# Performance work log

Hardware: AMD Instinct MI355X
Metric: run time of the kernel (lower is better)

Reference implementation:

```python
import jax, jax.numpy as jnp
import numpy as np

EMBED_DIM = 1024
NUM_HEADS = 16
BATCH = 4
SEQ = 4096


def setup_inputs() -> dict:
    key = jax.random.key(0)
    ks = jax.random.split(key, 5)
    scale = 0.02
    E = EMBED_DIM
    x = jax.random.normal(ks[0], (BATCH, SEQ, E), dtype=jnp.float32)
    Wq = jax.random.normal(ks[1], (E, E), dtype=jnp.float32) * scale
    Wk = jax.random.normal(ks[2], (E, E), dtype=jnp.float32) * scale
    Wv = jax.random.normal(ks[3], (E, E), dtype=jnp.float32) * scale
    Wo = jax.random.normal(ks[4], (E, E), dtype=jnp.float32) * scale
    z = jnp.zeros((E,), dtype=jnp.float32)
    return {"x": x, "Wq": Wq, "bq": z, "Wk": Wk, "bk": z, "Wv": Wv, "bv": z, "Wo": Wo, "bo": z}


def reference(x, Wq, bq, Wk, bk, Wv, bv, Wo, bo):
    B, S, E = x.shape
    H = NUM_HEADS
    D = E // H
    # torch nn.Linear: y = x @ W.T + b
    def proj(W, b):
        return (jnp.einsum('bse,fe->bsf', x, W) + b).reshape(B, S, H, D)
    q = jax.nn.elu(proj(Wq, bq)) + 1.0  # [B,S,H,D] feature map
    k = jax.nn.elu(proj(Wk, bk)) + 1.0
    v = proj(Wv, bv)
    # kv aggregation over sequence: [B,H,D,D]
    kv = jnp.einsum('bshd,bshe->bhde', k, v)
    # Q . KV: [B,S,H,D] -> merge heads -> [B,S,E]
    out = jnp.einsum('bshd,bhde->bshe', q, kv).reshape(B, S, E)
    # output projection (dropout is identity at inference)
    out = jnp.einsum('bse,fe->bsf', out, Wo) + bo
    return out
```

## Files before the change

### kernel.cpp

```cpp
#include <hip/hip_runtime.h>
#include <hip/hip_bf16.h>
#include <cstdint>
#include <cstddef>

#define BATCH 4
#define SEQ   4096
#define EMB   1024
#define M_TOT (BATCH * SEQ)
#define KV_CHUNKS 16

using bf16_t = __hip_bfloat16;
typedef __attribute__((ext_vector_type(8))) short bv8;
typedef __attribute__((ext_vector_type(4))) float f32x4;

union SV8 { bv8 v; bf16_t h[8]; };

__device__ __forceinline__ void gload_lds16(const void* g, void* l) {
  __builtin_amdgcn_global_load_lds(
      (const __attribute__((address_space(1))) unsigned int*)g,
      (__attribute__((address_space(3))) unsigned int*)l, 16, 0, 0);
}

#define BAR() asm volatile("s_barrier" ::: "memory")

__global__ __launch_bounds__(256) void cvt_kernel(const float* __restrict__ in,
                                                  bf16_t* __restrict__ out) {
  const size_t i = ((size_t)blockIdx.x * 256 + threadIdx.x) * 8;
  const f32x4 a = *(const f32x4*)(in + i);
  const f32x4 b = *(const f32x4*)(in + i + 4);
  SV8 o;
#pragma unroll
  for (int j = 0; j < 4; ++j) o.h[j] = __float2bfloat16(a[j]);
#pragma unroll
  for (int j = 0; j < 4; ++j) o.h[4 + j] = __float2bfloat16(b[j]);
  *(bv8*)(out + i) = o.v;
}

__global__ __launch_bounds__(256) void wcvt_kernel(
    const float* __restrict__ s0, const float* __restrict__ s1,
    const float* __restrict__ s2, const float* __restrict__ s3,
    bf16_t* __restrict__ d0, bf16_t* __restrict__ d1,
    bf16_t* __restrict__ d2, bf16_t* __restrict__ d3) {
  const float* in; bf16_t* out;
  switch (blockIdx.y) {
    case 0:  in = s0; out = d0; break;
    case 1:  in = s1; out = d1; break;
    case 2:  in = s2; out = d2; break;
    default: in = s3; out = d3; break;
  }
  const size_t i = ((size_t)blockIdx.x * 256 + threadIdx.x) * 8;
  const f32x4 a = *(const f32x4*)(in + i);
  const f32x4 b = *(const f32x4*)(in + i + 4);
  SV8 o;
#pragma unroll
  for (int j = 0; j < 4; ++j) o.h[j] = __float2bfloat16(a[j]);
#pragma unroll
  for (int j = 0; j < 4; ++j) o.h[4 + j] = __float2bfloat16(b[j]);
  *(bv8*)(out + i) = o.v;
}

template <int VARIANT>
__global__ __launch_bounds__(512, 2) void gemm8p(
    const bf16_t* __restrict__ A, const bf16_t* __restrict__ Wbase,
    const float* __restrict__ b0, const float* __restrict__ b1,
    const float* __restrict__ b2, void* __restrict__ o0,
    void* __restrict__ o1, void* __restrict__ o2) {
  constexpr int K = 1024;
  constexpr int NT = (VARIANT == 0) ? 12 : 4;
  constexpr int NKT = K / 64;
  __shared__ char lds[131072];

  const int nwg = NT * 64;
  const int wg = (blockIdx.x & 7) * (nwg >> 3) + (blockIdx.x >> 3);
  const int m0 = (wg / NT) * 256;
  const int n0 = (wg % NT) * 256;
  const bf16_t* W = Wbase + (VARIANT ? (size_t)(m0 >> 12) * 1048576ull : 0);
  const int t = threadIdx.x, l = t & 63, w = t >> 6;
  const int wm = w >> 2, wn = w & 3;

  const int sr = ((t >> 7) << 4) + (t & 15);
  const int sc = (((t >> 6) & 1) << 5) + (((t >> 4) & 3) << 3);
  const bf16_t* aRow = A + (size_t)(m0 + sr) * K + sc;
  const bf16_t* wRow = W + (size_t)(n0 + sr) * K + sc;
  char* dA = lds + t * 16;
  char* dB = lds + 65536 + t * 16;

  auto ST = [&](int isB, int hf, int kt) {
    char* d = (isB ? dB : dA) + (kt & 1) * 32768 + hf * 16384;
    const bf16_t* s = (isB ? wRow : aRow) + (size_t)(hf * 128) * K + kt * 64;
    gload_lds16(s, d);
    gload_lds16(s + (size_t)64 * K, d + 8192);
  };

  const char* Ab = lds + wm * 16384 + l * 16;
  const char* Bb = lds + 65536 + (wn >> 1) * 16384 + (wn & 1) * 8192 + l * 16;

  f32x4 acc[8][4] = {};
  bv8 af[4][2], bf[4][2];

  ST(1, 0, 0); ST(1, 1, 0); ST(0, 0, 0); ST(0, 1, 0);
  ST(1, 0, 1); ST(1, 1, 1); ST(0, 0, 1);
  asm volatile("s_waitcnt vmcnt(6)" ::: "memory");
  BAR();

#pragma unroll 1
  for (int j = 0; j < NKT; ++j) {
    const int db = (j & 1) * 32768;
#pragma unroll
    for (int mb = 0; mb < 4; ++mb)
#pragma unroll
      for (int ks = 0; ks < 2; ++ks)
        af[mb][ks] = *(const bv8*)(Ab + db + mb * 2048 + ks * 1024);
#pragma unroll
    for (int nb = 0; nb < 4; ++nb)
#pragma unroll
      for (int ks = 0; ks < 2; ++ks)
        bf[nb][ks] = *(const bv8*)(Bb + db + nb * 2048 + ks * 1024);
    if (j + 1 < NKT) ST(0, 1, j + 1);
    BAR();
    __builtin_amdgcn_s_setprio(1);
#pragma unroll
    for (int mb = 0; mb < 4; ++mb)
#pragma unroll
      for (int nb = 0; nb < 2; ++nb)
#pragma unroll
        for (int ks = 0; ks < 2; ++ks)
          acc[mb][nb] = __builtin_amdgcn_mfma_f32_16x16x32_bf16(
              af[mb][ks], bf[nb][ks], acc[mb][nb], 0, 0, 0);
    __builtin_amdgcn_s_setprio(0);
    BAR();
    if (j + 2 < NKT) ST(1, 0, j + 2);
    BAR();
    __builtin_amdgcn_s_setprio(1);
#pragma unroll
    for (int mb = 0; mb < 4; ++mb)
#pragma unroll
      for (int nb = 2; nb < 4; ++nb)
#pragma unroll
        for (int ks = 0; ks < 2; ++ks)
          acc[mb][nb] = __builtin_amdgcn_mfma_f32_16x16x32_bf16(
              af[mb][ks], bf[nb][ks], acc[mb][nb], 0, 0, 0);
    __builtin_amdgcn_s_setprio(0);
    BAR();
#pragma unroll
    for (int mb = 0; mb < 4; ++mb)
#pragma unroll
      for (int ks = 0; ks < 2; ++ks)
        af[mb][ks] = *(const bv8*)(Ab + db + 8192 + mb * 2048 + ks * 1024);
    if (j + 2 < NKT) ST(1, 1, j + 2);
    BAR();
    __builtin_amdgcn_s_setprio(1);
#pragma unroll
    for (int mb = 0; mb < 4; ++mb)
#pragma unroll
      for (int nb = 2; nb < 4; ++nb)
#pragma unroll
        for (int ks = 0; ks < 2; ++ks)
          acc[4 + mb][nb] = __builtin_amdgcn_mfma_f32_16x16x32_bf16(
              af[mb][ks], bf[nb][ks], acc[4 + mb][nb], 0, 0, 0);
    __builtin_amdgcn_s_setprio(0);
    BAR();
    if (j + 2 < NKT) {
      ST(0, 0, j + 2);
      asm volatile("s_waitcnt vmcnt(6)" ::: "memory");
    } else if (j == NKT - 2) {
      asm volatile("s_waitcnt vmcnt(0)" ::: "memory");
    }
    BAR();
    __builtin_amdgcn_s_setprio(1);
#pragma unroll
    for (int mb = 0; mb < 4; ++mb)
#pragma unroll
      for (int nb = 0; nb < 2; ++nb)
#pragma unroll
        for (int ks = 0; ks < 2; ++ks)
          acc[4 + mb][nb] = __builtin_amdgcn_mfma_f32_16x16x32_bf16(
              af[mb][ks], bf[nb][ks], acc[4 + mb][nb], 0, 0, 0);
    __builtin_amdgcn_s_setprio(0);
    BAR();
  }

  const int cr = (l >> 4) << 2, cc = l & 15;
  if (VARIANT == 0) {
    const int gq = n0 >> 10;
    const float* bias = gq == 0 ? b0 : (gq == 1 ? b1 : b2);
    bf16_t* ob = (bf16_t*)(gq == 0 ? o0 : (gq == 1 ? o1 : o2));
    const int cb = (n0 & 1023) + wn * 64;
#pragma unroll
    for (int nb = 0; nb < 4; ++nb) {
      const int col = cb + nb * 16 + cc;
      const float bz = bias[col];
#pragma unroll
      for (int mb = 0; mb < 8; ++mb) {
        const int row = m0 + wm * 128 + mb * 16 + cr;
#pragma unroll
        for (int r = 0; r < 4; ++r) {
          float v = acc[mb][nb][r] + bz;
          if (gq < 2) v = (v > 0.f) ? (v + 1.f) : __expf(v);
          ob[(size_t)(row + r) * 1024 + col] = __float2bfloat16(v);
        }
      }
    }
  } else {
    const int cb = n0 + wn * 64;
#pragma unroll
    for (int nb = 0; nb < 4; ++nb) {
      const int col = cb + nb * 16 + cc;
      const float bz = b0[col];
#pragma unroll
      for (int mb = 0; mb < 8; ++mb) {
        const int row = m0 + wm * 128 + mb * 16 + cr;
#pragma unroll
        for (int r = 0; r < 4; ++r)
          ((float*)o0)[(size_t)(row + r) * 1024 + col] = acc[mb][nb][r] + bz;
      }
    }
  }
}

__global__ __launch_bounds__(256) void kv_partial(const bf16_t* __restrict__ Kmat,
                                                  const bf16_t* __restrict__ Vmat,
                                                  float* __restrict__ pkv) {
  const int chunk = blockIdx.x;
  const int bh = blockIdx.y;
  const int b = bh >> 4, h = bh & 15;
  const int t = threadIdx.x;
  __shared__ bf16_t kl[8][64], vl[8][64];
  float acc[16] = {};
  const int e = t & 63, d0 = (t >> 6) * 16;
  const int sl = t >> 5, c2 = (t & 31) * 2;
  const int s0 = chunk * (SEQ / KV_CHUNKS);
  const bf16_t* kp = Kmat + ((size_t)(b * SEQ + s0 + sl)) * EMB + h * 64 + c2;
  const bf16_t* vp = Vmat + ((size_t)(b * SEQ + s0 + sl)) * EMB + h * 64 + c2;
  for (int it = 0; it < (SEQ / KV_CHUNKS) / 8; ++it) {
    const unsigned int kw = *(const unsigned int*)kp;
    const unsigned int vw = *(const unsigned int*)vp;
    __syncthreads();
    *(unsigned int*)&kl[sl][c2] = kw;
    *(unsigned int*)&vl[sl][c2] = vw;
    __syncthreads();
#pragma unroll
    for (int ss = 0; ss < 8; ++ss) {
      const float vv = __bfloat162float(vl[ss][e]);
      SV8 k0, k1;
      k0.v = *(const bv8*)&kl[ss][d0];
      k1.v = *(const bv8*)&kl[ss][d0 + 8];
#pragma unroll
      for (int dd = 0; dd < 8; ++dd) acc[dd] += __bfloat162float(k0.h[dd]) * vv;
#pragma unroll
      for (int dd = 0; dd < 8; ++dd) acc[8 + dd] += __bfloat162float(k1.h[dd]) * vv;
    }
    kp += 8 * EMB;
    vp += 8 * EMB;
  }
  float* outp = pkv + ((size_t)chunk * 64 + bh) * 4096;
#pragma unroll
  for (int dd = 0; dd < 16; ++dd) outp[(d0 + dd) * 64 + e] = acc[dd];
}

__global__ __launch_bounds__(256) void kv_reduce(const float* __restrict__ pkv,
                                                 bf16_t* __restrict__ kvf) {
  const int bh = blockIdx.x;
  const int t = threadIdx.x;
#pragma unroll
  for (int ii = 0; ii < 16; ++ii) {
    const int idx = ii * 256 + t;
    float s = 0.f;
#pragma unroll
    for (int c = 0; c < KV_CHUNKS; ++c)
      s += pkv[((size_t)c * 64 + bh) * 4096 + idx];
    kvf[(size_t)bh * 4096 + idx] = __float2bfloat16(s);
  }
}

__global__ __launch_bounds__(256) void fold_kernel(const bf16_t* __restrict__ Wo,
                                                   const bf16_t* __restrict__ kvf,
                                                   bf16_t* __restrict__ MT) {
  __shared__ char lds[24576];
  const int ft = blockIdx.x;
  const int bh = blockIdx.y;
  const int b = bh >> 4, h = bh & 15;
  const int t = threadIdx.x, l = t & 63, w = t >> 6;
#pragma unroll
  for (int q = 0; q < 4; ++q) {
    const int s = q * 256 + t;
    const int row = ((s >> 7) << 4) + (s & 15);
    const int col = (((s >> 6) & 1) << 5) + (((s >> 4) & 3) << 3);
    gload_lds16(Wo + (size_t)(ft * 128 + row) * 1024 + h * 64 + col, lds + s * 16);
  }
#pragma unroll
  for (int q = 0; q < 2; ++q) {
    const int s = q * 256 + t;
    const int row = ((s >> 7) << 4) + (s & 15);
    const int col = (((s >> 6) & 1) << 5) + (((s >> 4) & 3) << 3);
    gload_lds16(kvf + (size_t)bh * 4096 + row * 64 + col, lds + 16384 + s * 16);
  }
  asm volatile("s_waitcnt vmcnt(0)" ::: "memory");
  BAR();
  f32x4 acc[2][4] = {};
#pragma unroll
  for (int ks = 0; ks < 2; ++ks) {
    bv8 am[2], bn[4];
#pragma unroll
    for (int i = 0; i < 2; ++i)
      am[i] = *(const bv8*)(lds + (w * 2 + i) * 2048 + ks * 1024 + l * 16);
#pragma unroll
    for (int nb = 0; nb < 4; ++nb)
      bn[nb] = *(const bv8*)(lds + 16384 + nb * 2048 + ks * 1024 + l * 16);
#pragma unroll
    for (int i = 0; i < 2; ++i)
#pragma unroll
      for (int nb = 0; nb < 4; ++nb)
        acc[i][nb] = __builtin_amdgcn_mfma_f32_16x16x32_bf16(am[i], bn[nb],
                                                             acc[i][nb], 0, 0, 0);
  }
  bf16_t* out = MT + (size_t)b * 1048576ull;
  const int cr = (l >> 4) << 2, cc = l & 15;
#pragma unroll
  for (int i = 0; i < 2; ++i)
#pragma unroll
    for (int nb = 0; nb < 4; ++nb)
#pragma unroll
      for (int r = 0; r < 4; ++r)
        out[(size_t)(ft * 128 + w * 32 + i * 16 + cr + r) * 1024 + h * 64 +
            nb * 16 + cc] = __float2bfloat16(acc[i][nb][r]);
}

extern "C" void kernel_launch(void* const* d_in, const int* in_sizes, int n_in,
                              void* d_out, int out_size, void* d_ws, size_t ws_size,
                              hipStream_t stream) {
  (void)in_sizes; (void)n_in; (void)out_size;
  const float* x  = (const float*)d_in[0];
  const float* Wq = (const float*)d_in[1];
  const float* bq = (const float*)d_in[2];
  const float* Wk = (const float*)d_in[3];
  const float* bk = (const float*)d_in[4];
  const float* Wv = (const float*)d_in[5];
  const float* bv = (const float*)d_in[6];
  const float* Wo = (const float*)d_in[7];
  const float* bo = (const float*)d_in[8];

  const size_t NEED = 72ull * 1024 * 1024;
  if (ws_size < NEED) return;

  char* p = (char*)d_ws;
  bf16_t* xb   = (bf16_t*)p;
  float*  pkv  = (float*)p;
  bf16_t* kvf  = (bf16_t*)(p + 16777216ull);
  bf16_t* MT   = (bf16_t*)(p + 17825792ull);
  bf16_t* wqkv = (bf16_t*)(p + 33554432ull);
  bf16_t* wob  = (bf16_t*)(p + 39845888ull);
  bf16_t* qb   = (bf16_t*)(p + 41943040ull);

  bf16_t* kb = (bf16_t*)d_out;
  bf16_t* vb = kb + 16777216ull;

  cvt_kernel<<<8192, 256, 0, stream>>>(x, xb);
  wcvt_kernel<<<dim3(512, 4), 256, 0, stream>>>(
      Wq, Wk, Wv, Wo, wqkv, wqkv + 1048576, wqkv + 2097152, wob);

  gemm8p<0><<<768, 512, 0, stream>>>(xb, wqkv, bq, bk, bv, qb, kb, vb);

  kv_partial<<<dim3(KV_CHUNKS, 64), 256, 0, stream>>>(kb, vb, pkv);
  kv_reduce<<<64, 256, 0, stream>>>(pkv, kvf);
  fold_kernel<<<dim3(8, 64), 256, 0, stream>>>(wob, kvf, MT);

  gemm8p<1><<<256, 512, 0, stream>>>(qb, MT, bo, nullptr, nullptr,
                                     d_out, nullptr, nullptr);
}
```

Baseline: 389.7 us.

## Fuse conversion kernels, merge kv reduce into fold, vectorize GEMM epilogue stores

Merges the x and weight fp32-to-bf16 conversions into a single launch, and fuses the KV chunk reduction into the Wo fold kernel so the reduced KV matrix stays in LDS instead of going through global memory. It swaps the MFMA operand order so each lane holds four consecutive columns, which lets the GEMM epilogues use 4-wide vector stores and vector bias loads instead of scalar strided stores. The cost is that the fold now runs on only 64 blocks that loop serially over 8 output tiles, which lowers parallelism for that stage.

```diff
diff --git a/kernel.cpp b/kernel.cpp
--- a/kernel.cpp
+++ b/kernel.cpp
@@ -12,8 +12,16 @@
 using bf16_t = __hip_bfloat16;
 typedef __attribute__((ext_vector_type(8))) short bv8;
 typedef __attribute__((ext_vector_type(4))) float f32x4;
+typedef __attribute__((ext_vector_type(4))) unsigned short us4;
 
 union SV8 { bv8 v; bf16_t h[8]; };
+
+static __device__ __forceinline__ unsigned short bfbits(float v) {
+  bf16_t b = __float2bfloat16(v);
+  unsigned short u;
+  __builtin_memcpy(&u, &b, 2);
+  return u;
+}
 
 __device__ __forceinline__ void gload_lds16(const void* g, void* l) {
   __builtin_amdgcn_global_load_lds(
@@ -23,32 +31,28 @@
 
 #define BAR() asm volatile("s_barrier" ::: "memory")
 
-__global__ __launch_bounds__(256) void cvt_kernel(const float* __restrict__ in,
-                                                  bf16_t* __restrict__ out) {
-  const size_t i = ((size_t)blockIdx.x * 256 + threadIdx.x) * 8;
-  const f32x4 a = *(const f32x4*)(in + i);
-  const f32x4 b = *(const f32x4*)(in + i + 4);
-  SV8 o;
-#pragma unroll
-  for (int j = 0; j < 4; ++j) o.h[j] = __float2bfloat16(a[j]);
-#pragma unroll
-  for (int j = 0; j < 4; ++j) o.h[4 + j] = __float2bfloat16(b[j]);
-  *(bv8*)(out + i) = o.v;
-}
-
-__global__ __launch_bounds__(256) void wcvt_kernel(
-    const float* __restrict__ s0, const float* __restrict__ s1,
-    const float* __restrict__ s2, const float* __restrict__ s3,
-    bf16_t* __restrict__ d0, bf16_t* __restrict__ d1,
-    bf16_t* __restrict__ d2, bf16_t* __restrict__ d3) {
-  const float* in; bf16_t* out;
-  switch (blockIdx.y) {
-    case 0:  in = s0; out = d0; break;
-    case 1:  in = s1; out = d1; break;
-    case 2:  in = s2; out = d2; break;
-    default: in = s3; out = d3; break;
-  }
-  const size_t i = ((size_t)blockIdx.x * 256 + threadIdx.x) * 8;
+__global__ __launch_bounds__(256) void cvt_all(
+    const float* __restrict__ x, const float* __restrict__ wq,
+    const float* __restrict__ wk, const float* __restrict__ wv,
+    const float* __restrict__ wo, bf16_t* __restrict__ xb,
+    bf16_t* __restrict__ wqkv, bf16_t* __restrict__ wob) {
+  const int bid = blockIdx.x;
+  const float* in;
+  bf16_t* out;
+  size_t base;
+  if (bid < 8192) {
+    in = x; out = xb; base = (size_t)bid * 2048;
+  } else {
+    const int q = (bid - 8192) >> 9, sub = (bid - 8192) & 511;
+    base = (size_t)sub * 2048;
+    switch (q) {
+      case 0:  in = wq; out = wqkv; break;
+      case 1:  in = wk; out = wqkv + 1048576; break;
+      case 2:  in = wv; out = wqkv + 2097152; break;
+      default: in = wo; out = wob; break;
+    }
+  }
+  const size_t i = base + (size_t)threadIdx.x * 8;
   const f32x4 a = *(const f32x4*)(in + i);
   const f32x4 b = *(const f32x4*)(in + i + 4);
   SV8 o;
@@ -126,7 +130,7 @@
 #pragma unroll
         for (int ks = 0; ks < 2; ++ks)
           acc[mb][nb] = __builtin_amdgcn_mfma_f32_16x16x32_bf16(
-              af[mb][ks], bf[nb][ks], acc[mb][nb], 0, 0, 0);
+              bf[nb][ks], af[mb][ks], acc[mb][nb], 0, 0, 0);
     __builtin_amdgcn_s_setprio(0);
     BAR();
     if (j + 2 < NKT) ST(1, 0, j + 2);
@@ -139,7 +143,7 @@
 #pragma unroll
         for (int ks = 0; ks < 2; ++ks)
           acc[mb][nb] = __builtin_amdgcn_mfma_f32_16x16x32_bf16(
-              af[mb][ks], bf[nb][ks], acc[mb][nb], 0, 0, 0);
+              bf[nb][ks], af[mb][ks], acc[mb][nb], 0, 0, 0);
     __builtin_amdgcn_s_setprio(0);
     BAR();
 #pragma unroll
@@ -157,7 +161,7 @@
 #pragma unroll
         for (int ks = 0; ks < 2; ++ks)
           acc[4 + mb][nb] = __builtin_amdgcn_mfma_f32_16x16x32_bf16(
-              af[mb][ks], bf[nb][ks], acc[4 + mb][nb], 0, 0, 0);
+              bf[nb][ks], af[mb][ks], acc[4 + mb][nb], 0, 0, 0);
     __builtin_amdgcn_s_setprio(0);
     BAR();
     if (j + 2 < NKT) {
@@ -175,12 +179,14 @@
 #pragma unroll
         for (int ks = 0; ks < 2; ++ks)
           acc[4 + mb][nb] = __builtin_amdgcn_mfma_f32_16x16x32_bf16(
-              af[mb][ks], bf[nb][ks], acc[4 + mb][nb], 0, 0, 0);
+              bf[nb][ks], af[mb][ks], acc[4 + mb][nb], 0, 0, 0);
     __builtin_amdgcn_s_setprio(0);
     BAR();
   }
 
-  const int cr = (l >> 4) << 2, cc = l & 15;
+  const int rl = l & 15;
+  const int c4 = (l >> 4) << 2;
+  const int rbase = m0 + wm * 128;
   if (VARIANT == 0) {
     const int gq = n0 >> 10;
     const float* bias = gq == 0 ? b0 : (gq == 1 ? b1 : b2);
@@ -188,31 +194,32 @@
     const int cb = (n0 & 1023) + wn * 64;
 #pragma unroll
     for (int nb = 0; nb < 4; ++nb) {
-      const int col = cb + nb * 16 + cc;
-      const float bz = bias[col];
+      const int coln = cb + nb * 16 + c4;
+      const f32x4 bz = *(const f32x4*)(bias + coln);
 #pragma unroll
       for (int mb = 0; mb < 8; ++mb) {
-        const int row = m0 + wm * 128 + mb * 16 + cr;
+        us4 pk;
 #pragma unroll
         for (int r = 0; r < 4; ++r) {
-          float v = acc[mb][nb][r] + bz;
+          float v = acc[mb][nb][r] + bz[r];
           if (gq < 2) v = (v > 0.f) ? (v + 1.f) : __expf(v);
-          ob[(size_t)(row + r) * 1024 + col] = __float2bfloat16(v);
+          pk[r] = bfbits(v);
         }
+        *(us4*)(ob + (size_t)(rbase + mb * 16 + rl) * 1024 + coln) = pk;
       }
     }
   } else {
     const int cb = n0 + wn * 64;
 #pragma unroll
     for (int nb = 0; nb < 4; ++nb) {
-      const int col = cb + nb * 16 + cc;
-      const float bz = b0[col];
+      const int coln = cb + nb * 16 + c4;
+      const f32x4 bz = *(const f32x4*)(b0 + coln);
 #pragma unroll
       for (int mb = 0; mb < 8; ++mb) {
-        const int row = m0 + wm * 128 + mb * 16 + cr;
-#pragma unroll
-        for (int r = 0; r < 4; ++r)
-          ((float*)o0)[(size_t)(row + r) * 1024 + col] = acc[mb][nb][r] + bz;
+        f32x4 ov;
+#pragma unroll
+        for (int r = 0; r < 4; ++r) ov[r] = acc[mb][nb][r] + bz[r];
+        *(f32x4*)((float*)o0 + (size_t)(rbase + mb * 16 + rl) * 1024 + coln) = ov;
       }
     }
   }
@@ -258,72 +265,84 @@
   for (int dd = 0; dd < 16; ++dd) outp[(d0 + dd) * 64 + e] = acc[dd];
 }
 
-__global__ __launch_bounds__(256) void kv_reduce(const float* __restrict__ pkv,
-                                                 bf16_t* __restrict__ kvf) {
+__global__ __launch_bounds__(256) void fold2(const float* __restrict__ pkv,
+                                             const bf16_t* __restrict__ Wo,
+                                             bf16_t* __restrict__ MT) {
+  __shared__ char lds[24576];
   const int bh = blockIdx.x;
-  const int t = threadIdx.x;
-#pragma unroll
-  for (int ii = 0; ii < 16; ++ii) {
-    const int idx = ii * 256 + t;
-    float s = 0.f;
-#pragma unroll
-    for (int c = 0; c < KV_CHUNKS; ++c)
-      s += pkv[((size_t)c * 64 + bh) * 4096 + idx];
-    kvf[(size_t)bh * 4096 + idx] = __float2bfloat16(s);
-  }
-}
-
-__global__ __launch_bounds__(256) void fold_kernel(const bf16_t* __restrict__ Wo,
-                                                   const bf16_t* __restrict__ kvf,
-                                                   bf16_t* __restrict__ MT) {
-  __shared__ char lds[24576];
-  const int ft = blockIdx.x;
-  const int bh = blockIdx.y;
   const int b = bh >> 4, h = bh & 15;
   const int t = threadIdx.x, l = t & 63, w = t >> 6;
-#pragma unroll
-  for (int q = 0; q < 4; ++q) {
-    const int s = q * 256 + t;
-    const int row = ((s >> 7) << 4) + (s & 15);
-    const int col = (((s >> 6) & 1) << 5) + (((s >> 4) & 3) << 3);
-    gload_lds16(Wo + (size_t)(ft * 128 + row) * 1024 + h * 64 + col, lds + s * 16);
-  }
-#pragma unroll
-  for (int q = 0; q < 2; ++q) {
-    const int s = q * 256 + t;
-    const int row = ((s >> 7) << 4) + (s & 15);
-    const int col = (((s >> 6) & 1) << 5) + (((s >> 4) & 3) << 3);
-    gload_lds16(kvf + (size_t)bh * 4096 + row * 64 + col, lds + 16384 + s * 16);
-  }
-  asm volatile("s_waitcnt vmcnt(0)" ::: "memory");
-  BAR();
-  f32x4 acc[2][4] = {};
-#pragma unroll
-  for (int ks = 0; ks < 2; ++ks) {
-    bv8 am[2], bn[4];
+
+  const int d = t >> 2, e0 = (t & 3) * 16;
+  float s[16] = {};
+#pragma unroll
+  for (int c = 0; c < KV_CHUNKS; ++c) {
+    const float* pp = pkv + ((size_t)c * 64 + bh) * 4096 + d * 64 + e0;
+#pragma unroll
+    for (int q = 0; q < 4; ++q) {
+      const f32x4 v = *(const f32x4*)(pp + q * 4);
+#pragma unroll
+      for (int r = 0; r < 4; ++r) s[q * 4 + r] += v[r];
+    }
+  }
+  SV8 p0, p1;
+#pragma unroll
+  for (int j = 0; j < 8; ++j) p0.h[j] = __float2bfloat16(s[j]);
+#pragma unroll
+  for (int j = 0; j < 8; ++j) p1.h[j] = __float2bfloat16(s[8 + j]);
+  const int fb0 = (d >> 4) * 2048 + (d & 15) * 16;
+  *(bv8*)(lds + fb0 + (e0 >> 5) * 1024 + ((e0 >> 3) & 3) * 256) = p0.v;
+  const int e1 = e0 + 8;
+  *(bv8*)(lds + fb0 + (e1 >> 5) * 1024 + ((e1 >> 3) & 3) * 256) = p1.v;
+  __syncthreads();
+
+  bv8 bn[4][2];
+#pragma unroll
+  for (int db = 0; db < 4; ++db)
+#pragma unroll
+    for (int ks = 0; ks < 2; ++ks)
+      bn[db][ks] = *(const bv8*)(lds + db * 2048 + ks * 1024 + l * 16);
+
+  bf16_t* outB = MT + (size_t)b * 1048576ull + h * 64;
+  const int rl = l & 15, c4 = (l >> 4) << 2;
+  for (int ft = 0; ft < 8; ++ft) {
+#pragma unroll
+    for (int q = 0; q < 4; ++q) {
+      const int sslot = q * 256 + t;
+      const int row = ((sslot >> 7) << 4) + (sslot & 15);
+      const int col = (((sslot >> 6) & 1) << 5) + (((sslot >> 4) & 3) << 3);
+      gload_lds16(Wo + (size_t)(ft * 128 + row) * 1024 + h * 64 + col,
+                  lds + 8192 + sslot * 16);
+    }
+    asm volatile("s_waitcnt vmcnt(0)" ::: "memory");
+    __syncthreads();
+    f32x4 acc[4][2] = {};
+    bv8 am[2][2];
 #pragma unroll
     for (int i = 0; i < 2; ++i)
-      am[i] = *(const bv8*)(lds + (w * 2 + i) * 2048 + ks * 1024 + l * 16);
-#pragma unroll
-    for (int nb = 0; nb < 4; ++nb)
-      bn[nb] = *(const bv8*)(lds + 16384 + nb * 2048 + ks * 1024 + l * 16);
+#pragma unroll
+      for (int ks = 0; ks < 2; ++ks)
+        am[i][ks] = *(const bv8*)(lds + 8192 + (w * 2 + i) * 2048 + ks * 1024 + l * 16);
+#pragma unroll
+    for (int db = 0; db < 4; ++db)
+#pragma unroll
+      for (int i = 0; i < 2; ++i)
+#pragma unroll
+        for (int ks = 0; ks < 2; ++ks)
+          acc[db][i] = __builtin_amdgcn_mfma_f32_16x16x32_bf16(
+              bn[db][ks], am[i][ks], acc[db][i], 0, 0, 0);
 #pragma unroll
     for (int i = 0; i < 2; ++i)
 #pragma unroll
-      for (int nb = 0; nb < 4; ++nb)
-        acc[i][nb] = __builtin_amdgcn_mfma_f32_16x16x32_bf16(am[i], bn[nb],
-                                                             acc[i][nb], 0, 0, 0);
-  }
-  bf16_t* out = MT + (size_t)b * 1048576ull;
-  const int cr = (l >> 4) << 2, cc = l & 15;
-#pragma unroll
-  for (int i = 0; i < 2; ++i)
-#pragma unroll
-    for (int nb = 0; nb < 4; ++nb)
-#pragma unroll
-      for (int r = 0; r < 4; ++r)
-        out[(size_t)(ft * 128 + w * 32 + i * 16 + cr + r) * 1024 + h * 64 +
-            nb * 16 + cc] = __float2bfloat16(acc[i][nb][r]);
+      for (int db = 0; db < 4; ++db) {
+        us4 pk;
+#pragma unroll
+        for (int r = 0; r < 4; ++r) pk[r] = bfbits(acc[db][i][r]);
+        const int f = ft * 128 + w * 32 + i * 16 + rl;
+        *(us4*)(outB + (size_t)f * 1024 + db * 16 + c4) = pk;
+      }
+    __syncthreads();
+  }
 }
 
 extern "C" void kernel_launch(void* const* d_in, const int* in_sizes, int n_in,
@@ -346,7 +365,6 @@
   char* p = (char*)d_ws;
   bf16_t* xb   = (bf16_t*)p;
   float*  pkv  = (float*)p;
-  bf16_t* kvf  = (bf16_t*)(p + 16777216ull);
   bf16_t* MT   = (bf16_t*)(p + 17825792ull);
   bf16_t* wqkv = (bf16_t*)(p + 33554432ull);
   bf16_t* wob  = (bf16_t*)(p + 39845888ull);
@@ -355,15 +373,12 @@
   bf16_t* kb = (bf16_t*)d_out;
   bf16_t* vb = kb + 16777216ull;
 
-  cvt_kernel<<<8192, 256, 0, stream>>>(x, xb);
-  wcvt_kernel<<<dim3(512, 4), 256, 0, stream>>>(
-      Wq, Wk, Wv, Wo, wqkv, wqkv + 1048576, wqkv + 2097152, wob);
+  cvt_all<<<10240, 256, 0, stream>>>(x, Wq, Wk, Wv, Wo, xb, wqkv, wob);
 
   gemm8p<0><<<768, 512, 0, stream>>>(xb, wqkv, bq, bk, bv, qb, kb, vb);
 
   kv_partial<<<dim3(KV_CHUNKS, 64), 256, 0, stream>>>(kb, vb, pkv);
-  kv_reduce<<<64, 256, 0, stream>>>(pkv, kvf);
-  fold_kernel<<<dim3(8, 64), 256, 0, stream>>>(wob, kvf, MT);
+  fold2<<<64, 256, 0, stream>>>(pkv, wob, MT);
 
   gemm8p<1><<<256, 512, 0, stream>>>(qb, MT, bo, nullptr, nullptr,
                                      d_out, nullptr, nullptr);
```

Measured after the change: 401.0 us. 2.9% more time.
